# Optimization experiments

Measured on AMD Instinct MI355X. Metric: run time of the kernel, lower is better.

The kernel has to match this reference:

```python
import jax, jax.numpy as jnp
import numpy as np

N_NODES = 50000


def _gcn_norm(edge_index, num_nodes):
    # add self loops, compute symmetric normalization D^-1/2 (A+I) D^-1/2
    loops = jnp.arange(num_nodes, dtype=edge_index.dtype)
    row = jnp.concatenate([edge_index[0], loops])
    col = jnp.concatenate([edge_index[1], loops])
    deg = jax.ops.segment_sum(jnp.ones_like(row, dtype=jnp.float32), col,
                              num_segments=num_nodes)
    dinv = jnp.where(deg > 0, jax.lax.rsqrt(deg), 0.0)
    norm = dinv[row] * dinv[col]  # [E']
    return row, col, norm


def _gcn_conv(x, W, b, row, col, norm, num_nodes):
    h = x @ W                       # [N, out] transform first (smaller dim)
    msg = h[row] * norm[:, None]    # gather along source nodes  [E', out]
    agg = jax.ops.segment_sum(msg, col, num_segments=num_nodes)  # scatter-add
    return agg + b


def setup_inputs() -> dict:
    key = jax.random.key(0)
    k1, k2, k3, k4 = jax.random.split(key, 4)
    x = jax.random.normal(k1, (N_NODES, 128), dtype=jnp.float32)
    edge_index = jax.random.randint(k2, (2, 800000), 0, N_NODES, dtype=jnp.int64)
    W1 = jax.random.normal(k3, (128, 128), dtype=jnp.float32) * (1.0 / np.sqrt(128))
    b1 = jnp.zeros((128,), dtype=jnp.float32)
    W2 = jax.random.normal(k4, (128, 16), dtype=jnp.float32) * (1.0 / np.sqrt(128))
    b2 = jnp.zeros((16,), dtype=jnp.float32)
    return {"x": x, "edge_index": edge_index, "W1": W1, "b1": b1, "W2": W2, "b2": b2}


def reference(x, edge_index, W1, b1, W2, b2):
    n = x.shape[0]
    row, col, norm = _gcn_norm(edge_index, n)
    h = _gcn_conv(x, W1, b1, row, col, norm, n)
    h = jax.nn.relu(h)
    h = _gcn_conv(h, W2, b2, row, col, norm, n)
    return jax.nn.log_softmax(h, axis=1)
```

## Files before the change

### kernel.cpp

```cpp
#include <hip/hip_runtime.h>
#include <math.h>

constexpr int N  = 50000;
constexpr int E  = 800000;
constexpr int F1 = 128;
constexpr int F2 = 16;
constexpr int BSHIFT  = 8;
constexpr int NBUCKET = (N + 255) >> BSHIFT;
constexpr int CHUNK   = 2048;
constexpr int NB_S    = (E + CHUNK - 1) / CHUNK;
constexpr int NB_G    = (N + 63) / 64;
constexpr int CAP     = 6144;

typedef unsigned short ushort_t;
typedef unsigned char  uchar_t;
typedef __bf16 bf16x8 __attribute__((ext_vector_type(8)));
typedef float  f32x4  __attribute__((ext_vector_type(4)));

static __device__ __forceinline__ float blo(unsigned u) { return __uint_as_float(u << 16); }
static __device__ __forceinline__ float bhi(unsigned u) { return __uint_as_float(u & 0xffff0000u); }
static __device__ __forceinline__ ushort_t to_bf(float f) { __bf16 h = (__bf16)f; return *(ushort_t*)&h; }


__global__ __launch_bounds__(256) void k_scatG1(const int* __restrict__ row,
                                                const int* __restrict__ col,
                                                int* __restrict__ cursor,
                                                unsigned* __restrict__ P,
                                                const float* __restrict__ W1,
                                                const float* __restrict__ x,
                                                uchar_t* __restrict__ h1q) {
    __shared__ ushort_t smem[F1 * 136];
    int t = threadIdx.x;

    if (blockIdx.x < NB_S) {
        int* hist = (int*)smem;
        int* cur  = hist + NBUCKET;
        if (t < NBUCKET) hist[t] = 0;
        __syncthreads();
        int base = blockIdx.x * CHUNK;
#pragma unroll
        for (int i = 0; i < CHUNK / 256; ++i) {
            int e = base + i * 256 + t;
            if (e < E) atomicAdd(&hist[col[e] >> BSHIFT], 1);
        }
        __syncthreads();
        if (t < NBUCKET) cur[t] = t * CAP + atomicAdd(&cursor[t], hist[t]);
        __syncthreads();
#pragma unroll
        for (int i = 0; i < CHUNK / 256; ++i) {
            int e = base + i * 256 + t;
            if (e < E) {
                int c = col[e];
                int pos = atomicAdd(&cur[c >> BSHIFT], 1);
                P[pos] = ((unsigned)row[e] << BSHIFT) | (unsigned)(c & 255);
            }
        }
        return;
    }

    int blk = blockIdx.x - NB_S;
    for (int i = t; i < F1 * F1; i += 256) {
        int k = i >> 7, n = i & 127;
        smem[n * 136 + k] = to_bf(W1[i]);
    }
    __syncthreads();

    int lane = t & 63, wv = t >> 6;
    int quad = lane >> 4, l15 = lane & 15;
    int arow = blk * 64 + wv * 16 + l15;
    int rclamp = min(arow, N - 1);
    f32x4 acc[8] = {};

#pragma unroll
    for (int kk = 0; kk < 4; ++kk) {
        int k0 = kk * 32 + quad * 8;
        const float* xp = x + (size_t)rclamp * F1 + k0;
        float4 u0 = *(const float4*)xp;
        float4 u1 = *(const float4*)(xp + 4);
        bf16x8 a;
        a[0] = (__bf16)u0.x; a[1] = (__bf16)u0.y; a[2] = (__bf16)u0.z; a[3] = (__bf16)u0.w;
        a[4] = (__bf16)u1.x; a[5] = (__bf16)u1.y; a[6] = (__bf16)u1.z; a[7] = (__bf16)u1.w;
#pragma unroll
        for (int ct = 0; ct < 8; ++ct) {
            bf16x8 b = *(const bf16x8*)&smem[(ct * 16 + l15) * 136 + k0];
            acc[ct] = __builtin_amdgcn_mfma_f32_16x16x32_bf16(a, b, acc[ct], 0, 0, 0);
        }
    }

    int orow0 = blk * 64 + wv * 16 + quad * 4;
#pragma unroll
    for (int r = 0; r < 4; ++r) {
        int orow = orow0 + r;
        if (orow < N) {
            unsigned d0 = __builtin_amdgcn_cvt_pk_fp8_f32(acc[0][r], acc[1][r], 0, false);
            d0 = __builtin_amdgcn_cvt_pk_fp8_f32(acc[2][r], acc[3][r], d0, true);
            unsigned d1 = __builtin_amdgcn_cvt_pk_fp8_f32(acc[4][r], acc[5][r], 0, false);
            d1 = __builtin_amdgcn_cvt_pk_fp8_f32(acc[6][r], acc[7][r], d1, true);
            uint2 pw; pw.x = d0; pw.y = d1;
            *(uint2*)(h1q + (size_t)orow * F1 + l15 * 8) = pw;
        }
    }
}

__global__ __launch_bounds__(512) void k_binFinal(const unsigned* __restrict__ P,
                                                  const int* __restrict__ cursor,
                                                  ushort_t* __restrict__ csr16,
                                                  int* __restrict__ seg_start,
                                                  int* __restrict__ counts,
                                                  float* __restrict__ dinv) {
    __shared__ unsigned eb[CAP];
    __shared__ int cnt[256];
    __shared__ int cur[256];
    __shared__ int wtot[4];
    int t = threadIdx.x;
    int b = blockIdx.x;
    int lo = b << BSHIFT;
    int n_nodes = min(256, N - lo);
    int m = cursor[b];
    if (t < 256) cnt[t] = 0;
    __syncthreads();
    const unsigned* Pb = P + (size_t)b * CAP;
    for (int k = t; k < m; k += 512) {
        unsigned u = Pb[k];
        eb[k] = u;
        atomicAdd(&cnt[u & 255], 1);
    }
    __syncthreads();
    int lane = t & 63, wid = t >> 6;
    int v = 0, incl = 0;
    if (t < 256) {
        v = cnt[t];
        incl = v;
#pragma unroll
        for (int d = 1; d < 64; d <<= 1) {
            int u = __shfl_up(incl, d, 64);
            if (lane >= d) incl += u;
        }
        if (lane == 63) wtot[wid] = incl;
    }
    __syncthreads();
    if (t < 256) {
        int wb = 0;
        for (int w = 0; w < wid; ++w) wb += wtot[w];
        int o = b * CAP + wb + incl - v;
        cur[t] = o;
        if (t < n_nodes) {
            seg_start[lo + t] = o;
            counts[lo + t] = v;
            dinv[lo + t] = rsqrtf((float)v + 1.f);
        }
    }
    __syncthreads();
    for (int k = t; k < m; k += 512) {
        unsigned u = eb[k];
        int pos = atomicAdd(&cur[u & 255], 1);
        csr16[pos] = (ushort_t)(u >> BSHIFT);
    }
}

__global__ __launch_bounds__(256) void k_gather1(const uchar_t* __restrict__ h1q,
                                                 const int* __restrict__ seg_start,
                                                 const int* __restrict__ counts,
                                                 const ushort_t* __restrict__ csr16,
                                                 const float* __restrict__ dinv,
                                                 const float* __restrict__ b1,
                                                 const float* __restrict__ W2,
                                                 ushort_t* __restrict__ h2s) {
    int t = threadIdx.x;
    int c = (blockIdx.x * 256 + t) >> 6;
    int lane = t & 63;
    int sub = lane & 15, q = lane >> 4;

    float4 W2reg[8];
    float  b1reg[8];
#pragma unroll
    for (int j = 0; j < 8; ++j) {
        int f = j * 16 + sub;
        W2reg[j] = *(const float4*)(W2 + f * F2 + q * 4);
        b1reg[j] = b1[f];
    }

    int s = seg_start[c], e = s + counts[c];
    float acc[8] = {0.f, 0.f, 0.f, 0.f, 0.f, 0.f, 0.f, 0.f};
    for (int base = s; base < e; base += 4) {
        int k = base + q;
        bool valid = k < e;
        int r = valid ? (int)csr16[k] : c;
        float w = valid ? dinv[r] : 0.f;
        uint2 u = *(const uint2*)(h1q + (size_t)r * F1 + sub * 8);
        acc[0] = fmaf(__builtin_amdgcn_cvt_f32_fp8(u.x, 0), w, acc[0]);
        acc[1] = fmaf(__builtin_amdgcn_cvt_f32_fp8(u.x, 1), w, acc[1]);
        acc[2] = fmaf(__builtin_amdgcn_cvt_f32_fp8(u.x, 2), w, acc[2]);
        acc[3] = fmaf(__builtin_amdgcn_cvt_f32_fp8(u.x, 3), w, acc[3]);
        acc[4] = fmaf(__builtin_amdgcn_cvt_f32_fp8(u.y, 0), w, acc[4]);
        acc[5] = fmaf(__builtin_amdgcn_cvt_f32_fp8(u.y, 1), w, acc[5]);
        acc[6] = fmaf(__builtin_amdgcn_cvt_f32_fp8(u.y, 2), w, acc[6]);
        acc[7] = fmaf(__builtin_amdgcn_cvt_f32_fp8(u.y, 3), w, acc[7]);
    }
    float dc = dinv[c];
    if (q == 0) {
        uint2 u = *(const uint2*)(h1q + (size_t)c * F1 + sub * 8);
        acc[0] = fmaf(__builtin_amdgcn_cvt_f32_fp8(u.x, 0), dc, acc[0]);
        acc[1] = fmaf(__builtin_amdgcn_cvt_f32_fp8(u.x, 1), dc, acc[1]);
        acc[2] = fmaf(__builtin_amdgcn_cvt_f32_fp8(u.x, 2), dc, acc[2]);
        acc[3] = fmaf(__builtin_amdgcn_cvt_f32_fp8(u.x, 3), dc, acc[3]);
        acc[4] = fmaf(__builtin_amdgcn_cvt_f32_fp8(u.y, 0), dc, acc[4]);
        acc[5] = fmaf(__builtin_amdgcn_cvt_f32_fp8(u.y, 1), dc, acc[5]);
        acc[6] = fmaf(__builtin_amdgcn_cvt_f32_fp8(u.y, 2), dc, acc[6]);
        acc[7] = fmaf(__builtin_amdgcn_cvt_f32_fp8(u.y, 3), dc, acc[7]);
    }
#pragma unroll
    for (int j = 0; j < 8; ++j) acc[j] += __shfl_xor(acc[j], 16);
#pragma unroll
    for (int j = 0; j < 8; ++j) acc[j] += __shfl_xor(acc[j], 32);

    float4 o2 = {0.f, 0.f, 0.f, 0.f};
#pragma unroll
    for (int j = 0; j < 8; ++j) {
        float h = fmaxf(fmaf(dc, acc[j], b1reg[j]), 0.f);
        o2.x = fmaf(h, W2reg[j].x, o2.x);
        o2.y = fmaf(h, W2reg[j].y, o2.y);
        o2.z = fmaf(h, W2reg[j].z, o2.z);
        o2.w = fmaf(h, W2reg[j].w, o2.w);
    }
#pragma unroll
    for (int m = 1; m < 16; m <<= 1) {
        o2.x += __shfl_xor(o2.x, m);
        o2.y += __shfl_xor(o2.y, m);
        o2.z += __shfl_xor(o2.z, m);
        o2.w += __shfl_xor(o2.w, m);
    }
    if (sub == 0) {
        uint2 pw;
        pw.x = (unsigned)to_bf(o2.x * dc) | ((unsigned)to_bf(o2.y * dc) << 16);
        pw.y = (unsigned)to_bf(o2.z * dc) | ((unsigned)to_bf(o2.w * dc) << 16);
        *(uint2*)(h2s + (size_t)c * F2 + q * 4) = pw;
    }
}

__global__ __launch_bounds__(256) void k_gather2(const ushort_t* __restrict__ h2s,
                                                 const int* __restrict__ seg_start,
                                                 const int* __restrict__ counts,
                                                 const ushort_t* __restrict__ csr16,
                                                 const float* __restrict__ dinv,
                                                 const float* __restrict__ b2,
                                                 float* __restrict__ out) {
    int idx = blockIdx.x * 256 + threadIdx.x;
    int node = idx >> 3, sub = idx & 7;
    if (node >= N) return;
    int s = seg_start[node], e = s + counts[node];
    float ax = 0.f, ay = 0.f;
    int k = s;
    for (; k + 4 <= e; k += 4) {
        int r0 = csr16[k], r1 = csr16[k + 1], r2 = csr16[k + 2], r3 = csr16[k + 3];
        unsigned u0 = ((const unsigned*)(h2s + (size_t)r0 * F2))[sub];
        unsigned u1 = ((const unsigned*)(h2s + (size_t)r1 * F2))[sub];
        unsigned u2 = ((const unsigned*)(h2s + (size_t)r2 * F2))[sub];
        unsigned u3 = ((const unsigned*)(h2s + (size_t)r3 * F2))[sub];
        ax += (blo(u0) + blo(u1)) + (blo(u2) + blo(u3));
        ay += (bhi(u0) + bhi(u1)) + (bhi(u2) + bhi(u3));
    }
    for (; k < e; ++k) {
        unsigned u = ((const unsigned*)(h2s + (size_t)csr16[k] * F2))[sub];
        ax += blo(u);
        ay += bhi(u);
    }
    unsigned us = ((const unsigned*)(h2s + (size_t)node * F2))[sub];
    ax += blo(us);
    ay += bhi(us);
    float dc = dinv[node];
    float2 bb = ((const float2*)b2)[sub];
    float v0 = fmaf(dc, ax, bb.x);
    float v1 = fmaf(dc, ay, bb.y);
    float mx = fmaxf(v0, v1);
#pragma unroll
    for (int m = 1; m < 8; m <<= 1) mx = fmaxf(mx, __shfl_xor(mx, m));
    float sm = expf(v0 - mx) + expf(v1 - mx);
#pragma unroll
    for (int m = 1; m < 8; m <<= 1) sm += __shfl_xor(sm, m);
    float lse = mx + logf(sm);
    float2 o;
    o.x = v0 - lse;
    o.y = v1 - lse;
    ((float2*)(out + (size_t)node * F2))[sub] = o;
}

extern "C" void kernel_launch(void* const* d_in, const int* in_sizes, int n_in,
                              void* d_out, int out_size, void* d_ws, size_t ws_size,
                              hipStream_t stream) {
    const float* x  = (const float*)d_in[0];
    const int*   ei = (const int*)d_in[1];
    const float* W1 = (const float*)d_in[2];
    const float* b1 = (const float*)d_in[3];
    const float* W2 = (const float*)d_in[4];
    const float* b2 = (const float*)d_in[5];
    const int* row = ei;
    const int* col = ei + E;

    char* ws = (char*)d_ws;
    int*      cursor    = (int*)ws;      ws += 256 * 4;
    unsigned* P         = (unsigned*)ws; ws += (size_t)NBUCKET * CAP * 4;
    ushort_t* csr16     = (ushort_t*)ws; ws += (size_t)(NBUCKET * CAP + 8) * 2;
    int*      seg_start = (int*)ws;      ws += (size_t)N * 4;
    int*      counts    = (int*)ws;      ws += (size_t)N * 4;
    float*    dinv      = (float*)ws;    ws += (size_t)N * 4;
    uchar_t*  h1q       = (uchar_t*)ws;  ws += (size_t)N * F1;
    ushort_t* h2s       = (ushort_t*)ws; ws += (size_t)N * F2 * 2;

    hipMemsetAsync(cursor, 0, 256 * 4, stream);

    k_scatG1<<<NB_S + NB_G, 256, 0, stream>>>(row, col, cursor, P, W1, x, h1q);
    k_binFinal<<<NBUCKET, 512, 0, stream>>>(P, cursor, csr16, seg_start, counts, dinv);
    k_gather1<<<(N * 64) / 256, 256, 0, stream>>>(h1q, seg_start, counts, csr16, dinv, b1, W2,
                                                  h2s);
    k_gather2<<<((size_t)N * 8 + 255) / 256, 256, 0, stream>>>(h2s, seg_start, counts, csr16,
                                                               dinv, b2, (float*)d_out);
}
```

Baseline: 173.7 us.

## Pre-scale GEMM1 output by source dinv to drop per-edge dinv gather

```diff
diff --git a/kernel.cpp b/kernel.cpp
--- a/kernel.cpp
+++ b/kernel.cpp
@@ -8,8 +8,6 @@
 constexpr int BSHIFT  = 8;
 constexpr int NBUCKET = (N + 255) >> BSHIFT;
 constexpr int CHUNK   = 2048;
-constexpr int NB_S    = (E + CHUNK - 1) / CHUNK;
-constexpr int NB_G    = (N + 63) / 64;
 constexpr int CAP     = 6144;
 
 typedef unsigned short ushort_t;
@@ -22,82 +20,31 @@
 static __device__ __forceinline__ ushort_t to_bf(float f) { __bf16 h = (__bf16)f; return *(ushort_t*)&h; }
 
 
-__global__ __launch_bounds__(256) void k_scatG1(const int* __restrict__ row,
-                                                const int* __restrict__ col,
-                                                int* __restrict__ cursor,
-                                                unsigned* __restrict__ P,
-                                                const float* __restrict__ W1,
-                                                const float* __restrict__ x,
-                                                uchar_t* __restrict__ h1q) {
-    __shared__ ushort_t smem[F1 * 136];
+__global__ __launch_bounds__(256) void k_scatP(const int* __restrict__ row,
+                                               const int* __restrict__ col,
+                                               int* __restrict__ cursor,
+                                               unsigned* __restrict__ P) {
+    __shared__ int hist[NBUCKET];
+    __shared__ int cur[NBUCKET];
     int t = threadIdx.x;
-
-    if (blockIdx.x < NB_S) {
-        int* hist = (int*)smem;
-        int* cur  = hist + NBUCKET;
-        if (t < NBUCKET) hist[t] = 0;
-        __syncthreads();
-        int base = blockIdx.x * CHUNK;
-#pragma unroll
-        for (int i = 0; i < CHUNK / 256; ++i) {
-            int e = base + i * 256 + t;
-            if (e < E) atomicAdd(&hist[col[e] >> BSHIFT], 1);
-        }
-        __syncthreads();
-        if (t < NBUCKET) cur[t] = t * CAP + atomicAdd(&cursor[t], hist[t]);
-        __syncthreads();
-#pragma unroll
-        for (int i = 0; i < CHUNK / 256; ++i) {
-            int e = base + i * 256 + t;
-            if (e < E) {
-                int c = col[e];
-                int pos = atomicAdd(&cur[c >> BSHIFT], 1);
-                P[pos] = ((unsigned)row[e] << BSHIFT) | (unsigned)(c & 255);
-            }
-        }
-        return;
-    }
-
-    int blk = blockIdx.x - NB_S;
-    for (int i = t; i < F1 * F1; i += 256) {
-        int k = i >> 7, n = i & 127;
-        smem[n * 136 + k] = to_bf(W1[i]);
-    }
-    __syncthreads();
-
-    int lane = t & 63, wv = t >> 6;
-    int quad = lane >> 4, l15 = lane & 15;
-    int arow = blk * 64 + wv * 16 + l15;
-    int rclamp = min(arow, N - 1);
-    f32x4 acc[8] = {};
-
-#pragma unroll
-    for (int kk = 0; kk < 4; ++kk) {
-        int k0 = kk * 32 + quad * 8;
-        const float* xp = x + (size_t)rclamp * F1 + k0;
-        float4 u0 = *(const float4*)xp;
-        float4 u1 = *(const float4*)(xp + 4);
-        bf16x8 a;
-        a[0] = (__bf16)u0.x; a[1] = (__bf16)u0.y; a[2] = (__bf16)u0.z; a[3] = (__bf16)u0.w;
-        a[4] = (__bf16)u1.x; a[5] = (__bf16)u1.y; a[6] = (__bf16)u1.z; a[7] = (__bf16)u1.w;
-#pragma unroll
-        for (int ct = 0; ct < 8; ++ct) {
-            bf16x8 b = *(const bf16x8*)&smem[(ct * 16 + l15) * 136 + k0];
-            acc[ct] = __builtin_amdgcn_mfma_f32_16x16x32_bf16(a, b, acc[ct], 0, 0, 0);
-        }
-    }
-
-    int orow0 = blk * 64 + wv * 16 + quad * 4;
-#pragma unroll
-    for (int r = 0; r < 4; ++r) {
-        int orow = orow0 + r;
-        if (orow < N) {
-            unsigned d0 = __builtin_amdgcn_cvt_pk_fp8_f32(acc[0][r], acc[1][r], 0, false);
-            d0 = __builtin_amdgcn_cvt_pk_fp8_f32(acc[2][r], acc[3][r], d0, true);
-            unsigned d1 = __builtin_amdgcn_cvt_pk_fp8_f32(acc[4][r], acc[5][r], 0, false);
-            d1 = __builtin_amdgcn_cvt_pk_fp8_f32(acc[6][r], acc[7][r], d1, true);
-            uint2 pw; pw.x = d0; pw.y = d1;
-            *(uint2*)(h1q + (size_t)orow * F1 + l15 * 8) = pw;
+    if (t < NBUCKET) hist[t] = 0;
+    __syncthreads();
+    int base = blockIdx.x * CHUNK;
+#pragma unroll
+    for (int i = 0; i < CHUNK / 256; ++i) {
+        int e = base + i * 256 + t;
+        if (e < E) atomicAdd(&hist[col[e] >> BSHIFT], 1);
+    }
+    __syncthreads();
+    if (t < NBUCKET) cur[t] = t * CAP + atomicAdd(&cursor[t], hist[t]);
+    __syncthreads();
+#pragma unroll
+    for (int i = 0; i < CHUNK / 256; ++i) {
+        int e = base + i * 256 + t;
+        if (e < E) {
+            int c = col[e];
+            int pos = atomicAdd(&cur[c >> BSHIFT], 1);
+            P[pos] = ((unsigned)row[e] << BSHIFT) | (unsigned)(c & 255);
         }
     }
 }
@@ -158,6 +105,56 @@
     }
 }
 
+__global__ __launch_bounds__(256) void k_gemm1(const float* __restrict__ x,
+                                               const float* __restrict__ W1,
+                                               const float* __restrict__ dinv,
+                                               uchar_t* __restrict__ h1q) {
+    __shared__ ushort_t smem[F1 * 136];
+    int t = threadIdx.x;
+    for (int i = t; i < F1 * F1; i += 256) {
+        int k = i >> 7, n = i & 127;
+        smem[n * 136 + k] = to_bf(W1[i]);
+    }
+    __syncthreads();
+
+    int lane = t & 63, wv = t >> 6;
+    int quad = lane >> 4, l15 = lane & 15;
+    int arow = blockIdx.x * 64 + wv * 16 + l15;
+    int rclamp = min(arow, N - 1);
+    f32x4 acc[8] = {};
+
+#pragma unroll
+    for (int kk = 0; kk < 4; ++kk) {
+        int k0 = kk * 32 + quad * 8;
+        const float* xp = x + (size_t)rclamp * F1 + k0;
+        float4 u0 = *(const float4*)xp;
+        float4 u1 = *(const float4*)(xp + 4);
+        bf16x8 a;
+        a[0] = (__bf16)u0.x; a[1] = (__bf16)u0.y; a[2] = (__bf16)u0.z; a[3] = (__bf16)u0.w;
+        a[4] = (__bf16)u1.x; a[5] = (__bf16)u1.y; a[6] = (__bf16)u1.z; a[7] = (__bf16)u1.w;
+#pragma unroll
+        for (int ct = 0; ct < 8; ++ct) {
+            bf16x8 b = *(const bf16x8*)&smem[(ct * 16 + l15) * 136 + k0];
+            acc[ct] = __builtin_amdgcn_mfma_f32_16x16x32_bf16(a, b, acc[ct], 0, 0, 0);
+        }
+    }
+
+    int orow0 = blockIdx.x * 64 + wv * 16 + quad * 4;
+#pragma unroll
+    for (int r = 0; r < 4; ++r) {
+        int orow = orow0 + r;
+        if (orow < N) {
+            float d = dinv[orow];
+            unsigned d0 = __builtin_amdgcn_cvt_pk_fp8_f32(acc[0][r] * d, acc[1][r] * d, 0, false);
+            d0 = __builtin_amdgcn_cvt_pk_fp8_f32(acc[2][r] * d, acc[3][r] * d, d0, true);
+            unsigned d1 = __builtin_amdgcn_cvt_pk_fp8_f32(acc[4][r] * d, acc[5][r] * d, 0, false);
+            d1 = __builtin_amdgcn_cvt_pk_fp8_f32(acc[6][r] * d, acc[7][r] * d, d1, true);
+            uint2 pw; pw.x = d0; pw.y = d1;
+            *(uint2*)(h1q + (size_t)orow * F1 + l15 * 8) = pw;
+        }
+    }
+}
+
 __global__ __launch_bounds__(256) void k_gather1(const uchar_t* __restrict__ h1q,
                                                  const int* __restrict__ seg_start,
                                                  const int* __restrict__ counts,
@@ -186,7 +183,7 @@
         int k = base + q;
         bool valid = k < e;
         int r = valid ? (int)csr16[k] : c;
-        float w = valid ? dinv[r] : 0.f;
+        float w = valid ? 1.f : 0.f;
         uint2 u = *(const uint2*)(h1q + (size_t)r * F1 + sub * 8);
         acc[0] = fmaf(__builtin_amdgcn_cvt_f32_fp8(u.x, 0), w, acc[0]);
         acc[1] = fmaf(__builtin_amdgcn_cvt_f32_fp8(u.x, 1), w, acc[1]);
@@ -197,23 +194,23 @@
         acc[6] = fmaf(__builtin_amdgcn_cvt_f32_fp8(u.y, 2), w, acc[6]);
         acc[7] = fmaf(__builtin_amdgcn_cvt_f32_fp8(u.y, 3), w, acc[7]);
     }
-    float dc = dinv[c];
     if (q == 0) {
         uint2 u = *(const uint2*)(h1q + (size_t)c * F1 + sub * 8);
-        acc[0] = fmaf(__builtin_amdgcn_cvt_f32_fp8(u.x, 0), dc, acc[0]);
-        acc[1] = fmaf(__builtin_amdgcn_cvt_f32_fp8(u.x, 1), dc, acc[1]);
-        acc[2] = fmaf(__builtin_amdgcn_cvt_f32_fp8(u.x, 2), dc, acc[2]);
-        acc[3] = fmaf(__builtin_amdgcn_cvt_f32_fp8(u.x, 3), dc, acc[3]);
-        acc[4] = fmaf(__builtin_amdgcn_cvt_f32_fp8(u.y, 0), dc, acc[4]);
-        acc[5] = fmaf(__builtin_amdgcn_cvt_f32_fp8(u.y, 1), dc, acc[5]);
-        acc[6] = fmaf(__builtin_amdgcn_cvt_f32_fp8(u.y, 2), dc, acc[6]);
-        acc[7] = fmaf(__builtin_amdgcn_cvt_f32_fp8(u.y, 3), dc, acc[7]);
+        acc[0] += __builtin_amdgcn_cvt_f32_fp8(u.x, 0);
+        acc[1] += __builtin_amdgcn_cvt_f32_fp8(u.x, 1);
+        acc[2] += __builtin_amdgcn_cvt_f32_fp8(u.x, 2);
+        acc[3] += __builtin_amdgcn_cvt_f32_fp8(u.x, 3);
+        acc[4] += __builtin_amdgcn_cvt_f32_fp8(u.y, 0);
+        acc[5] += __builtin_amdgcn_cvt_f32_fp8(u.y, 1);
+        acc[6] += __builtin_amdgcn_cvt_f32_fp8(u.y, 2);
+        acc[7] += __builtin_amdgcn_cvt_f32_fp8(u.y, 3);
     }
 #pragma unroll
     for (int j = 0; j < 8; ++j) acc[j] += __shfl_xor(acc[j], 16);
 #pragma unroll
     for (int j = 0; j < 8; ++j) acc[j] += __shfl_xor(acc[j], 32);
 
+    float dc = dinv[c];
     float4 o2 = {0.f, 0.f, 0.f, 0.f};
 #pragma unroll
     for (int j = 0; j < 8; ++j) {
@@ -309,8 +306,9 @@
 
     hipMemsetAsync(cursor, 0, 256 * 4, stream);
 
-    k_scatG1<<<NB_S + NB_G, 256, 0, stream>>>(row, col, cursor, P, W1, x, h1q);
+    k_scatP<<<(E + CHUNK - 1) / CHUNK, 256, 0, stream>>>(row, col, cursor, P);
     k_binFinal<<<NBUCKET, 512, 0, stream>>>(P, cursor, csr16, seg_start, counts, dinv);
+    k_gemm1<<<(N + 63) / 64, 256, 0, stream>>>(x, W1, dinv, h1q);
     k_gather1<<<(N * 64) / 256, 256, 0, stream>>>(h1q, seg_start, counts, csr16, dinv, b1, W2,
                                                   h2s);
     k_gather2<<<((size_t)N * 8 + 255) / 256, 256, 0, stream>>>(h2s, seg_start, counts, csr16,
```

Measured after the change: 179.7 us. 1.03x slower.
